# Optimization experiments

Hardware: AMD Instinct MI355X
Metric: run time of the kernel (lower is better)

The kernel has to match this reference:

```python
import jax, jax.numpy as jnp
import numpy as np

H = 4           # attention heads
NEG_SLOPE = 0.2 # GATConv default leaky_relu slope
BN_EPS = 1e-5


def gat_conv(x, src, dst, W, a_src, a_dst, b, N):
    # PyG GATConv (concat=True, add_self_loops=True): self-loops appended by caller.
    C = W.shape[1] // H
    h = (x @ W).reshape(N, H, C)                      # [N,H,C]
    al_s = jnp.einsum('nhc,hc->nh', h, a_src)          # [N,H]
    al_d = jnp.einsum('nhc,hc->nh', h, a_dst)
    e = jax.nn.leaky_relu(al_s[src] + al_d[dst], NEG_SLOPE)   # [E,H]
    m = jax.ops.segment_max(e, dst, num_segments=N)            # per-dst softmax (stable)
    p = jnp.exp(e - m[dst])
    s = jax.ops.segment_sum(p, dst, num_segments=N)
    alpha = p / s[dst]                                          # [E,H]
    out = jax.ops.segment_sum(alpha[:, :, None] * h[src], dst, num_segments=N)  # [N,H,C]
    return out.reshape(N, H * C) + b


def mp_layer(x, src, dst, gw, gas, gad, gb, fw, fb, fg, fbeta, N):
    gat_out = gat_conv(x, src, dst, gw, gas, gad, gb, N)
    # feature_transform: Linear -> BatchNorm1d (eval: running_mean=0, running_var=1) -> ReLU
    y = x @ fw + fb
    y = y * (fg / jnp.sqrt(1.0 + BN_EPS)) + fbeta
    y = jax.nn.relu(y)
    return gat_out + y


def forward(x, edge_index, edge_attr, params):
    N = x.shape[0]
    loop = jnp.arange(N, dtype=edge_index.dtype)
    src = jnp.concatenate([edge_index[0], loop])   # add self loops (GATConv default)
    dst = jnp.concatenate([edge_index[1], loop])
    for p in params[:-1]:
        x = mp_layer(x, src, dst, *p, N)
        x = jax.nn.relu(x)   # dropout is identity in eval mode
    cw, cb = params[-1]
    return x @ cw + cb


def setup_inputs() -> dict:
    N, E, D, Hd, O = 80000, 1000000, 512, 128, 10
    key = jax.random.key(0)
    ks = jax.random.split(key, 40)
    ki = iter(range(40))

    def rn(shape, fan_in):
        return jax.random.normal(ks[next(ki)], shape, dtype=jnp.float32) / np.sqrt(fan_in)

    inp = {}
    inp['x'] = jax.random.normal(ks[next(ki)], (N, D), dtype=jnp.float32)
    inp['edge_index'] = jax.random.randint(ks[next(ki)], (2, E), 0, N, dtype=jnp.int64)
    inp['edge_attr'] = jax.random.uniform(ks[next(ki)], (E, 1), dtype=jnp.float32)
    dims = [D, Hd, Hd]
    for li, din in enumerate(dims):
        inp[f'l{li}_gw'] = rn((din, Hd), din)
        inp[f'l{li}_gas'] = rn((H, Hd // H), Hd // H)
        inp[f'l{li}_gad'] = rn((H, Hd // H), Hd // H)
        inp[f'l{li}_gb'] = jnp.zeros((Hd,), jnp.float32)
        inp[f'l{li}_fw'] = rn((din, Hd), din)
        inp[f'l{li}_fb'] = jnp.zeros((Hd,), jnp.float32)
        inp[f'l{li}_fg'] = jnp.ones((Hd,), jnp.float32)
        inp[f'l{li}_fbeta'] = jnp.zeros((Hd,), jnp.float32)
    inp['cls_w'] = rn((Hd, O), Hd)
    inp['cls_b'] = jnp.zeros((O,), jnp.float32)
    return inp


def reference(x, edge_index, edge_attr,
              l0_gw, l0_gas, l0_gad, l0_gb, l0_fw, l0_fb, l0_fg, l0_fbeta,
              l1_gw, l1_gas, l1_gad, l1_gb, l1_fw, l1_fb, l1_fg, l1_fbeta,
              l2_gw, l2_gas, l2_gad, l2_gb, l2_fw, l2_fb, l2_fg, l2_fbeta,
              cls_w, cls_b):
    params = [
        (l0_gw, l0_gas, l0_gad, l0_gb, l0_fw, l0_fb, l0_fg, l0_fbeta),
        (l1_gw, l1_gas, l1_gad, l1_gb, l1_fw, l1_fb, l1_fg, l1_fbeta),
        (l2_gw, l2_gas, l2_gad, l2_gb, l2_fw, l2_fb, l2_fg, l2_fbeta),
        (cls_w, cls_b),
    ]
    return forward(x, edge_index, edge_attr, params)
```

## Files before the change

kernel.cpp:

```cpp
#include <hip/hip_runtime.h>
#include <cstdint>
#include <cstddef>

#define HD 128
#define NEG_SLOPE 0.2f
#define BN_EPS 1e-5f

typedef __bf16 bf16x8 __attribute__((ext_vector_type(8)));
typedef float  f32x4  __attribute__((ext_vector_type(4)));

__device__ __forceinline__ unsigned short f2b(float f) {
    unsigned int u = __float_as_uint(f);
    u = (u + 0x7fffu + ((u >> 16) & 1u)) >> 16;
    return (unsigned short)u;
}
__device__ __forceinline__ unsigned int pack2(float lo, float hi) {
    return (unsigned int)f2b(lo) | ((unsigned int)f2b(hi) << 16);
}

__device__ __forceinline__ void gload_lds16(const void* g, void* l) {
    __builtin_amdgcn_global_load_lds(
        (const __attribute__((address_space(1))) uint32_t*)g,
        (__attribute__((address_space(3))) uint32_t*)l, 16, 0, 0);
}

__global__ void prep_w2(const float* __restrict__ gw, const float* __restrict__ fw,
                        unsigned short* __restrict__ Wt, int K)
{
    int t = blockIdx.x * 256 + threadIdx.x;
    if (t >= K * 256) return;
    int k = t >> 8, c = t & 255;
    float v = (c < 128) ? gw[(size_t)k * 128 + c] : fw[(size_t)k * 128 + (c - 128)];
    Wt[(size_t)c * K + k] = f2b(v);
}

__global__ __launch_bounds__(256, 4) void gemm_dual(
    const float* __restrict__ X, const unsigned short* __restrict__ Wt,
    unsigned short* __restrict__ hb, float* __restrict__ yb, int M, int K,
    const float* __restrict__ fb, const float* __restrict__ fg,
    const float* __restrict__ fbeta, const float* __restrict__ gb)
{
    __shared__ __align__(16) char smem[64 * 128 + 256 * 64];
    char* Asb = smem;
    char* Bsb = smem + 64 * 128;

    const int tid  = threadIdx.x;
    const int lane = tid & 63, w = tid >> 6;
    const int row0 = blockIdx.x * 64;
    const int m = lane & 15, q = lane >> 4;

    const int la = lane >> 3, ca = lane & 7;
    const int lb = lane >> 2, cb = lane & 3;
    const int oA = 4 * (ca ^ la);
    const int oB = 8 * (cb ^ (la & 3));

    const float* ap[2];
    const unsigned short* bp[4];
#pragma unroll
    for (int i = 0; i < 2; i++) {
        int r  = (i * 4 + w) * 8 + la;
        int gr = row0 + r; if (gr >= M) gr = M - 1;
        ap[i] = X + (size_t)gr * K + oA;
    }
#pragma unroll
    for (int i = 0; i < 4; i++) {
        int r = (i * 4 + w) * 16 + lb;
        bp[i] = Wt + (size_t)r * K + oB;
    }

    f32x4 acc[4][4];
#pragma unroll
    for (int rt = 0; rt < 4; rt++)
#pragma unroll
        for (int ct = 0; ct < 4; ct++) acc[rt][ct] = (f32x4){0.f, 0.f, 0.f, 0.f};

    for (int ks = 0; ks < K; ks += 32) {
        __syncthreads();
#pragma unroll
        for (int i = 0; i < 2; i++)
            gload_lds16(ap[i] + ks, Asb + (i * 4 + w) * 1024);
#pragma unroll
        for (int i = 0; i < 4; i++)
            gload_lds16(bp[i] + ks, Bsb + (i * 4 + w) * 1024);
        __syncthreads();

        bf16x8 af[4], bfr[4];
#pragma unroll
        for (int rt = 0; rt < 4; rt++) {
            int row = rt * 16 + m;
            const char* base = Asb + (row << 7);
            int sw = (m & 7) << 4;
            f32x4 a0 = *(const f32x4*)(base + ((q * 32)      ^ sw));
            f32x4 a1 = *(const f32x4*)(base + ((q * 32 + 16) ^ sw));
            uint4 av;
            av.x = pack2(a0.x, a0.y); av.y = pack2(a0.z, a0.w);
            av.z = pack2(a1.x, a1.y); av.w = pack2(a1.z, a1.w);
            af[rt] = *(bf16x8*)&av;
        }
#pragma unroll
        for (int ct = 0; ct < 4; ct++) {
            int row = w * 64 + ct * 16 + m;
            bfr[ct] = *(const bf16x8*)(Bsb + (row << 6) +
                                       ((q * 16) ^ (((m >> 1) & 3) << 4)));
        }
#pragma unroll
        for (int rt = 0; rt < 4; rt++)
#pragma unroll
            for (int ct = 0; ct < 4; ct++)
                acc[rt][ct] = __builtin_amdgcn_mfma_f32_16x16x32_bf16(af[rt], bfr[ct], acc[rt][ct], 0, 0, 0);
    }

    if (w < 2) {
#pragma unroll
        for (int ct = 0; ct < 4; ct++) {
            int col = 64 * w + ct * 16 + m;
#pragma unroll
            for (int rt = 0; rt < 4; rt++)
#pragma unroll
                for (int r = 0; r < 4; r++) {
                    int row = row0 + rt * 16 + q * 4 + r;
                    if (row < M) hb[(size_t)row * HD + col] = f2b(acc[rt][ct][r]);
                }
        }
    } else {
        const float inv_bn = 1.0f / sqrtf(1.0f + BN_EPS);
#pragma unroll
        for (int ct = 0; ct < 4; ct++) {
            int col = 64 * (w - 2) + ct * 16 + m;
            float g  = fg[col] * inv_bn;
            float bb = fb[col];
            float bt = fbeta[col];
            float gv = gb[col];
#pragma unroll
            for (int rt = 0; rt < 4; rt++)
#pragma unroll
                for (int r = 0; r < 4; r++) {
                    int row = row0 + rt * 16 + q * 4 + r;
                    if (row < M) {
                        float y = (acc[rt][ct][r] + bb) * g + bt;
                        y = y > 0.f ? y : 0.f;
                        yb[(size_t)row * HD + col] = y + gv;
                    }
                }
        }
    }
}

__global__ void al_kernel(const unsigned short* __restrict__ h,
                          const float* __restrict__ a_src, const float* __restrict__ a_dst,
                          float* __restrict__ als, float* __restrict__ ald, int N)
{
    int t = blockIdx.x * blockDim.x + threadIdx.x;
    if (t >= N * 4) return;
    int n = t >> 2, hd = t & 3;
    const unsigned short* hp = h + (size_t)n * HD + hd * 32;
    const float* as = a_src + hd * 32;
    const float* ad = a_dst + hd * 32;
    float s1 = 0.f, s2 = 0.f;
#pragma unroll
    for (int i = 0; i < 32; i += 8) {
        uint4 hv = *(const uint4*)(hp + i);
        unsigned int u[4] = {hv.x, hv.y, hv.z, hv.w};
#pragma unroll
        for (int p = 0; p < 4; p++) {
            float f0 = __uint_as_float(u[p] << 16);
            float f1 = __uint_as_float(u[p] & 0xffff0000u);
            s1 += f0 * as[i + 2 * p] + f1 * as[i + 2 * p + 1];
            s2 += f0 * ad[i + 2 * p] + f1 * ad[i + 2 * p + 1];
        }
    }
    als[t] = s1; ald[t] = s2;
}

__global__ void hist_kernel(const int* __restrict__ ei, int E, int N, int* __restrict__ deg)
{
    int t = blockIdx.x * blockDim.x + threadIdx.x;
    if (t >= E + N) return;
    int d = (t < E) ? ei[E + t] : (t - E);
    atomicAdd(&deg[d], 1);
}

__global__ void scan1(const int* __restrict__ deg, int* __restrict__ rp,
                      int* __restrict__ bsum, int N)
{
    __shared__ int sh[256];
    int t = threadIdx.x;
    int i0 = blockIdx.x * 1024 + t * 4;
    int v[4];
#pragma unroll
    for (int j = 0; j < 4; j++) v[j] = (i0 + j < N) ? deg[i0 + j] : 0;
    int tot = v[0] + v[1] + v[2] + v[3];
    sh[t] = tot;
    __syncthreads();
    for (int off = 1; off < 256; off <<= 1) {
        int xv = (t >= off) ? sh[t - off] : 0;
        __syncthreads();
        sh[t] += xv;
        __syncthreads();
    }
    int run = sh[t] - tot;
    if (t == 255) bsum[blockIdx.x] = sh[255];
#pragma unroll
    for (int j = 0; j < 4; j++) {
        if (i0 + j < N) rp[i0 + j] = run;
        run += v[j];
    }
}

__global__ void scan2(int* __restrict__ bsum, int nb)
{
    if (threadIdx.x == 0 && blockIdx.x == 0) {
        int run = 0;
        for (int i = 0; i < nb; i++) { int v = bsum[i]; bsum[i] = run; run += v; }
    }
}

__global__ void scan3(int* __restrict__ rp, int* __restrict__ cur,
                      const int* __restrict__ bsum, int N, int Etot)
{
    int t = blockIdx.x * blockDim.x + threadIdx.x;
    if (t < N) {
        int v = rp[t] + bsum[t >> 10];
        rp[t] = v;
        cur[t] = v;
    } else if (t == N) {
        rp[N] = Etot;
    }
}

__global__ void scatter_kernel(const int* __restrict__ ei, int E, int N,
                               int* __restrict__ cur, int* __restrict__ col)
{
    int t = blockIdx.x * blockDim.x + threadIdx.x;
    if (t >= E + N) return;
    int s, d;
    if (t < E) { s = ei[t]; d = ei[E + t]; } else { s = t - E; d = t - E; }
    int p = atomicAdd(&cur[d], 1);
    col[p] = s;
}

__global__ __launch_bounds__(256) void agg_kernel(
    const unsigned short* __restrict__ h, const float* __restrict__ als,
    const float* __restrict__ ald, const int* __restrict__ rp,
    const int* __restrict__ col, float* __restrict__ xio, int N)
{
    int wid  = (blockIdx.x * blockDim.x + threadIdx.x) >> 6;
    int lane = threadIdx.x & 63;
    if (wid >= N) return;
    int beg = rp[wid], end = rp[wid + 1];

    int g = lane >> 4, c = lane & 15, hB = c >> 2;
    float ad_h = ald[wid * 4 + hB];
    float acc[8];
#pragma unroll
    for (int p = 0; p < 8; p++) acc[p] = 0.f;
    float wsum = 0.f;
    const unsigned short* hbase = h + c * 8;
    for (int j = beg + g; j < end; j += 4) {
        int s = col[j];
        float e = als[s * 4 + hB] + ad_h;
        e = e > 0.f ? e : NEG_SLOPE * e;
        float wgt = __expf(e);
        wsum += wgt;
        uint4 hv = *(const uint4*)(hbase + (size_t)s * HD);
        unsigned int uu[4] = {hv.x, hv.y, hv.z, hv.w};
#pragma unroll
        for (int p = 0; p < 4; p++) {
            acc[2 * p]     += wgt * __uint_as_float(uu[p] << 16);
            acc[2 * p + 1] += wgt * __uint_as_float(uu[p] & 0xffff0000u);
        }
    }
#pragma unroll
    for (int p = 0; p < 8; p++) {
        acc[p] += __shfl_xor(acc[p], 16);
        acc[p] += __shfl_xor(acc[p], 32);
    }
    wsum += __shfl_xor(wsum, 16);
    wsum += __shfl_xor(wsum, 32);
    if (g == 0) {
        float inv = 1.0f / wsum;
        float* xp = xio + (size_t)wid * HD + c * 8;
        float4 x0 = *(float4*)xp, x1 = *(float4*)(xp + 4);
        float o[8] = {acc[0] * inv + x0.x, acc[1] * inv + x0.y,
                      acc[2] * inv + x0.z, acc[3] * inv + x0.w,
                      acc[4] * inv + x1.x, acc[5] * inv + x1.y,
                      acc[6] * inv + x1.z, acc[7] * inv + x1.w};
#pragma unroll
        for (int p = 0; p < 8; p++) o[p] = o[p] > 0.f ? o[p] : 0.f;
        *(float4*)xp       = (float4){o[0], o[1], o[2], o[3]};
        *(float4*)(xp + 4) = (float4){o[4], o[5], o[6], o[7]};
    }
}

__global__ __launch_bounds__(256) void cls_kernel(
    const float* __restrict__ x, const float* __restrict__ w,
    const float* __restrict__ b, float* __restrict__ out, int N)
{
    int wid  = (blockIdx.x * blockDim.x + threadIdx.x) >> 6;
    int lane = threadIdx.x & 63;
    if (wid >= N) return;
    float x0 = x[(size_t)wid * HD + lane];
    float x1 = x[(size_t)wid * HD + 64 + lane];
    float acc[10];
#pragma unroll
    for (int o = 0; o < 10; o++)
        acc[o] = x0 * w[lane * 10 + o] + x1 * w[(lane + 64) * 10 + o];
#pragma unroll
    for (int o = 0; o < 10; o++) {
        float v = acc[o];
#pragma unroll
        for (int off = 1; off < 64; off <<= 1) v += __shfl_xor(v, off);
        acc[o] = v;
    }
    float v = 0.f;
#pragma unroll
    for (int o = 0; o < 10; o++) if (lane == o) v = acc[o];
    if (lane < 10) out[(size_t)wid * 10 + lane] = v + b[lane];
}

extern "C" void kernel_launch(void* const* d_in, const int* in_sizes, int n_in,
                              void* d_out, int out_size, void* d_ws, size_t ws_size,
                              hipStream_t stream)
{
    const float* x0 = (const float*)d_in[0];
    const int*   ei = (const int*)d_in[1];
    const int N = in_sizes[0] / 512;
    const int E = in_sizes[1] / 2;
    const int Etot = E + N;

    const float *gw[3], *gas[3], *gad[3], *gbp[3], *fw[3], *fbp[3], *fgp[3], *fbt[3];
    for (int l = 0; l < 3; l++) {
        int b = 3 + 8 * l;
        gw[l]  = (const float*)d_in[b + 0];
        gas[l] = (const float*)d_in[b + 1];
        gad[l] = (const float*)d_in[b + 2];
        gbp[l] = (const float*)d_in[b + 3];
        fw[l]  = (const float*)d_in[b + 4];
        fbp[l] = (const float*)d_in[b + 5];
        fgp[l] = (const float*)d_in[b + 6];
        fbt[l] = (const float*)d_in[b + 7];
    }
    const float* cw = (const float*)d_in[27];
    const float* cb = (const float*)d_in[28];

    char* p = (char*)d_ws;
    auto carve = [&](size_t bytes) -> char* {
        char* r = p; p += (bytes + 255) & ~(size_t)255; return r;
    };
    float* xA   = (float*)carve((size_t)N * HD * 4);
    float* xB   = (float*)carve((size_t)N * HD * 4);
    unsigned short* hbuf = (unsigned short*)carve((size_t)N * HD * 2);
    float* als  = (float*)carve((size_t)N * 4 * 4);
    float* ald  = (float*)carve((size_t)N * 4 * 4);
    int* rp   = (int*)carve((size_t)(N + 1) * 4);
    int* deg  = (int*)carve((size_t)N * 4);
    int* cur  = (int*)carve((size_t)N * 4);
    int* bsum = (int*)carve(4096);
    int* col  = (int*)carve((size_t)Etot * 4);
    unsigned short* wT[3];
    for (int l = 0; l < 3; l++) {
        int K = (l == 0) ? 512 : HD;
        wT[l] = (unsigned short*)carve((size_t)256 * K * 2);
    }

    for (int l = 0; l < 3; l++) {
        int K = (l == 0) ? 512 : HD;
        int nt = K * 256;
        prep_w2<<<(nt + 255) / 256, 256, 0, stream>>>(gw[l], fw[l], wT[l], K);
    }

    hipMemsetAsync(deg, 0, (size_t)N * 4, stream);
    hist_kernel<<<(Etot + 255) / 256, 256, 0, stream>>>(ei, E, N, deg);
    int nb = (N + 1023) / 1024;
    scan1<<<nb, 256, 0, stream>>>(deg, rp, bsum, N);
    scan2<<<1, 64, 0, stream>>>(bsum, nb);
    scan3<<<(N + 256) / 256, 256, 0, stream>>>(rp, cur, bsum, N, Etot);
    scatter_kernel<<<(Etot + 255) / 256, 256, 0, stream>>>(ei, E, N, cur, col);

    for (int l = 0; l < 3; l++) {
        const float* xin = (l == 0) ? x0 : ((l == 1) ? xA : xB);
        float* xout = (l == 1) ? xB : xA;
        int K = (l == 0) ? 512 : HD;
        int mblocks = (N + 63) / 64;
        gemm_dual<<<mblocks, 256, 0, stream>>>(xin, wT[l], hbuf, xout, N, K,
                                               fbp[l], fgp[l], fbt[l], gbp[l]);
        al_kernel<<<(N * 4 + 255) / 256, 256, 0, stream>>>(hbuf, gas[l], gad[l], als, ald, N);
        agg_kernel<<<(N + 3) / 4, 256, 0, stream>>>(hbuf, als, ald, rp, col, xout, N);
    }

    cls_kernel<<<(N + 3) / 4, 256, 0, stream>>>(xA, cw, cb, (float*)d_out, N);
}
```

Baseline: 791.2 us.

## Load GEMM operands directly to registers with double buffering; widen agg lanes

The dual GEMM no longer stages X and W tiles through LDS with global_load_lds and barriers. Each lane now loads its MFMA fragments straight from global memory into registers, using a two-stage software pipeline that overlaps the next K-slice load with the current MFMAs. Occupancy is lowered to 2 blocks per CU to make room for the extra registers. Separately, the aggregation kernel gives each lane 16 channels (two uint4 loads) and handles 8 edges in parallel per wavefront instead of 4, which adds one more shuffle reduction step.

```diff
diff --git a/kernel.cpp b/kernel.cpp
--- a/kernel.cpp
+++ b/kernel.cpp
@@ -16,12 +16,6 @@
 }
 __device__ __forceinline__ unsigned int pack2(float lo, float hi) {
     return (unsigned int)f2b(lo) | ((unsigned int)f2b(hi) << 16);
-}
-
-__device__ __forceinline__ void gload_lds16(const void* g, void* l) {
-    __builtin_amdgcn_global_load_lds(
-        (const __attribute__((address_space(1))) uint32_t*)g,
-        (__attribute__((address_space(3))) uint32_t*)l, 16, 0, 0);
 }
 
 __global__ void prep_w2(const float* __restrict__ gw, const float* __restrict__ fw,
@@ -34,38 +28,55 @@
     Wt[(size_t)c * K + k] = f2b(v);
 }
 
-__global__ __launch_bounds__(256, 4) void gemm_dual(
+#define LOADT(pa0, pa1, pb, OFF)                                              \
+    _Pragma("unroll") for (int rt = 0; rt < 4; rt++) {                        \
+        pa0[rt] = *(const float4*)(xr[rt] + (OFF));                           \
+        pa1[rt] = *(const float4*)(xr[rt] + (OFF) + 4);                       \
+    }                                                                         \
+    _Pragma("unroll") for (int ct = 0; ct < 4; ct++)                          \
+        pb[ct] = *(const uint4*)(wr[ct] + (OFF));
+
+#define COMPUTET(pa0, pa1, pb)                                                \
+    {                                                                         \
+        bf16x8 af[4], bfr[4];                                                 \
+        _Pragma("unroll") for (int rt = 0; rt < 4; rt++) {                    \
+            uint4 av;                                                         \
+            av.x = pack2(pa0[rt].x, pa0[rt].y);                               \
+            av.y = pack2(pa0[rt].z, pa0[rt].w);                               \
+            av.z = pack2(pa1[rt].x, pa1[rt].y);                               \
+            av.w = pack2(pa1[rt].z, pa1[rt].w);                               \
+            af[rt] = *(bf16x8*)&av;                                           \
+        }                                                                     \
+        _Pragma("unroll") for (int ct = 0; ct < 4; ct++)                      \
+            bfr[ct] = *(bf16x8*)&pb[ct];                                      \
+        _Pragma("unroll") for (int rt = 0; rt < 4; rt++)                      \
+            _Pragma("unroll") for (int ct = 0; ct < 4; ct++)                  \
+                acc[rt][ct] = __builtin_amdgcn_mfma_f32_16x16x32_bf16(        \
+                    af[rt], bfr[ct], acc[rt][ct], 0, 0, 0);                   \
+    }
+
+__global__ __launch_bounds__(256, 2) void gemm_dual(
     const float* __restrict__ X, const unsigned short* __restrict__ Wt,
     unsigned short* __restrict__ hb, float* __restrict__ yb, int M, int K,
     const float* __restrict__ fb, const float* __restrict__ fg,
     const float* __restrict__ fbeta, const float* __restrict__ gb)
 {
-    __shared__ __align__(16) char smem[64 * 128 + 256 * 64];
-    char* Asb = smem;
-    char* Bsb = smem + 64 * 128;
-
     const int tid  = threadIdx.x;
     const int lane = tid & 63, w = tid >> 6;
     const int row0 = blockIdx.x * 64;
     const int m = lane & 15, q = lane >> 4;
 
-    const int la = lane >> 3, ca = lane & 7;
-    const int lb = lane >> 2, cb = lane & 3;
-    const int oA = 4 * (ca ^ la);
-    const int oB = 8 * (cb ^ (la & 3));
-
-    const float* ap[2];
-    const unsigned short* bp[4];
-#pragma unroll
-    for (int i = 0; i < 2; i++) {
-        int r  = (i * 4 + w) * 8 + la;
-        int gr = row0 + r; if (gr >= M) gr = M - 1;
-        ap[i] = X + (size_t)gr * K + oA;
-    }
-#pragma unroll
-    for (int i = 0; i < 4; i++) {
-        int r = (i * 4 + w) * 16 + lb;
-        bp[i] = Wt + (size_t)r * K + oB;
+    const float* xr[4];
+    const unsigned short* wr[4];
+#pragma unroll
+    for (int rt = 0; rt < 4; rt++) {
+        int gr = row0 + rt * 16 + m; if (gr >= M) gr = M - 1;
+        xr[rt] = X + (size_t)gr * K + q * 8;
+    }
+#pragma unroll
+    for (int ct = 0; ct < 4; ct++) {
+        int n = w * 64 + ct * 16 + m;
+        wr[ct] = Wt + (size_t)n * K + q * 8;
     }
 
     f32x4 acc[4][4];
@@ -74,40 +85,14 @@
 #pragma unroll
         for (int ct = 0; ct < 4; ct++) acc[rt][ct] = (f32x4){0.f, 0.f, 0.f, 0.f};
 
-    for (int ks = 0; ks < K; ks += 32) {
-        __syncthreads();
-#pragma unroll
-        for (int i = 0; i < 2; i++)
-            gload_lds16(ap[i] + ks, Asb + (i * 4 + w) * 1024);
-#pragma unroll
-        for (int i = 0; i < 4; i++)
-            gload_lds16(bp[i] + ks, Bsb + (i * 4 + w) * 1024);
-        __syncthreads();
-
-        bf16x8 af[4], bfr[4];
-#pragma unroll
-        for (int rt = 0; rt < 4; rt++) {
-            int row = rt * 16 + m;
-            const char* base = Asb + (row << 7);
-            int sw = (m & 7) << 4;
-            f32x4 a0 = *(const f32x4*)(base + ((q * 32)      ^ sw));
-            f32x4 a1 = *(const f32x4*)(base + ((q * 32 + 16) ^ sw));
-            uint4 av;
-            av.x = pack2(a0.x, a0.y); av.y = pack2(a0.z, a0.w);
-            av.z = pack2(a1.x, a1.y); av.w = pack2(a1.z, a1.w);
-            af[rt] = *(bf16x8*)&av;
-        }
-#pragma unroll
-        for (int ct = 0; ct < 4; ct++) {
-            int row = w * 64 + ct * 16 + m;
-            bfr[ct] = *(const bf16x8*)(Bsb + (row << 6) +
-                                       ((q * 16) ^ (((m >> 1) & 3) << 4)));
-        }
-#pragma unroll
-        for (int rt = 0; rt < 4; rt++)
-#pragma unroll
-            for (int ct = 0; ct < 4; ct++)
-                acc[rt][ct] = __builtin_amdgcn_mfma_f32_16x16x32_bf16(af[rt], bfr[ct], acc[rt][ct], 0, 0, 0);
+    float4 pA0[4], pA1[4]; uint4 pB[4];
+    float4 qA0[4], qA1[4]; uint4 qB[4];
+    LOADT(pA0, pA1, pB, 0);
+    for (int ks = 0; ks < K; ks += 64) {
+        LOADT(qA0, qA1, qB, ks + 32);
+        COMPUTET(pA0, pA1, pB);
+        if (ks + 64 < K) { LOADT(pA0, pA1, pB, ks + 64); }
+        COMPUTET(qA0, qA1, qB);
     }
 
     if (w < 2) {
@@ -249,46 +234,53 @@
     if (wid >= N) return;
     int beg = rp[wid], end = rp[wid + 1];
 
-    int g = lane >> 4, c = lane & 15, hB = c >> 2;
+    int g = lane >> 3, c = lane & 7, hB = c >> 1;
     float ad_h = ald[wid * 4 + hB];
-    float acc[8];
-#pragma unroll
-    for (int p = 0; p < 8; p++) acc[p] = 0.f;
+    float acc[16];
+#pragma unroll
+    for (int p = 0; p < 16; p++) acc[p] = 0.f;
     float wsum = 0.f;
-    const unsigned short* hbase = h + c * 8;
-    for (int j = beg + g; j < end; j += 4) {
+    const unsigned short* hbase = h + c * 16;
+    for (int j = beg + g; j < end; j += 8) {
         int s = col[j];
         float e = als[s * 4 + hB] + ad_h;
         e = e > 0.f ? e : NEG_SLOPE * e;
         float wgt = __expf(e);
         wsum += wgt;
-        uint4 hv = *(const uint4*)(hbase + (size_t)s * HD);
-        unsigned int uu[4] = {hv.x, hv.y, hv.z, hv.w};
-#pragma unroll
-        for (int p = 0; p < 4; p++) {
+        const uint4* hp = (const uint4*)(hbase + (size_t)s * HD);
+        uint4 hv0 = hp[0], hv1 = hp[1];
+        unsigned int uu[8] = {hv0.x, hv0.y, hv0.z, hv0.w,
+                              hv1.x, hv1.y, hv1.z, hv1.w};
+#pragma unroll
+        for (int p = 0; p < 8; p++) {
             acc[2 * p]     += wgt * __uint_as_float(uu[p] << 16);
             acc[2 * p + 1] += wgt * __uint_as_float(uu[p] & 0xffff0000u);
         }
     }
 #pragma unroll
-    for (int p = 0; p < 8; p++) {
+    for (int p = 0; p < 16; p++) {
+        acc[p] += __shfl_xor(acc[p], 8);
         acc[p] += __shfl_xor(acc[p], 16);
         acc[p] += __shfl_xor(acc[p], 32);
     }
+    wsum += __shfl_xor(wsum, 8);
     wsum += __shfl_xor(wsum, 16);
     wsum += __shfl_xor(wsum, 32);
     if (g == 0) {
         float inv = 1.0f / wsum;
-        float* xp = xio + (size_t)wid * HD + c * 8;
-        float4 x0 = *(float4*)xp, x1 = *(float4*)(xp + 4);
-        float o[8] = {acc[0] * inv + x0.x, acc[1] * inv + x0.y,
-                      acc[2] * inv + x0.z, acc[3] * inv + x0.w,
-                      acc[4] * inv + x1.x, acc[5] * inv + x1.y,
-                      acc[6] * inv + x1.z, acc[7] * inv + x1.w};
-#pragma unroll
-        for (int p = 0; p < 8; p++) o[p] = o[p] > 0.f ? o[p] : 0.f;
-        *(float4*)xp       = (float4){o[0], o[1], o[2], o[3]};
-        *(float4*)(xp + 4) = (float4){o[4], o[5], o[6], o[7]};
+        float* xp = xio + (size_t)wid * HD + c * 16;
+        float4 xv[4];
+#pragma unroll
+        for (int b = 0; b < 4; b++) xv[b] = *(float4*)(xp + 4 * b);
+        float o[16];
+#pragma unroll
+        for (int p = 0; p < 16; p++) {
+            float t = acc[p] * inv + ((float*)xv)[p];
+            o[p] = t > 0.f ? t : 0.f;
+        }
+#pragma unroll
+        for (int b = 0; b < 4; b++)
+            *(float4*)(xp + 4 * b) = (float4){o[4*b], o[4*b+1], o[4*b+2], o[4*b+3]};
     }
 }
 
```

New measurement: 878.7 us. +11.1%, slower.
